# Optimization experiments

Hardware: AMD Instinct MI355X
Metric: run time of the kernel (lower is better)

## Reference

```python
import jax, jax.numpy as jnp
import numpy as np

NUM_HEADS = 12
CF = 2            # compression_factor
DEPTH = 3
BLOCK_DEPTH = 2
TOTAL_DEPTH_M1 = 14 - 1


def setup_inputs() -> dict:
    key = jax.random.key(0)
    k1, k2, k3, k4 = jax.random.split(key, 4)
    B, N, C = 64, 577, 768
    x = jax.random.normal(k1, (B, N, C), dtype=jnp.float32)
    qkv_w = jax.random.normal(k2, (3 * C, C), dtype=jnp.float32) * (C ** -0.5)
    proj_w = jax.random.normal(k3, (C, C), dtype=jnp.float32) * (C ** -0.5)
    proj_b = jax.random.normal(k4, (C,), dtype=jnp.float32) * 0.02
    return {"x": x, "qkv_w": qkv_w, "proj_w": proj_w, "proj_b": proj_b}


def _attn_branch(xh, qkv_w, proj_w, proj_b, zero_small):
    Bh, N, C = xh.shape
    H = NUM_HEADS
    D = C // H
    scale = D ** -0.5
    # qkv projection (no bias), split into q,k,v of shape [Bh, H, N, D]
    qkv = jnp.einsum('bnc,oc->bno', xh, qkv_w)  # [Bh, N, 3C]
    qkv = qkv.reshape(Bh, N, 3, H, D).transpose(2, 0, 3, 1, 4)  # [3, Bh, H, N, D]
    if zero_small:
        # statically zero compressed heads in q, k, v (as the torch in-place write does)
        qkv = qkv.at[:, :, H // CF:].set(0.0)
    q, k, v = qkv[0], qkv[1], qkv[2]
    attn = jnp.einsum('bhnd,bhmd->bhnm', q, k) * scale
    attn = jax.nn.softmax(attn, axis=-1)
    out = jnp.einsum('bhnm,bhmd->bhnd', attn, v)
    out = out.transpose(0, 2, 1, 3).reshape(Bh, N, C)
    out = jnp.einsum('bnc,oc->bno', out, proj_w) + proj_b
    if zero_small:
        out = out.at[:, :, C // CF:].set(0.0)
    return out


def reference(x, qkv_w, proj_w, proj_b):
    B = x.shape[0]
    x_large = _attn_branch(x[:B // 2], qkv_w, proj_w, proj_b, zero_small=False)
    if BLOCK_DEPTH <= DEPTH <= TOTAL_DEPTH_M1 - BLOCK_DEPTH:
        x_small = _attn_branch(x[B // 2:], qkv_w, proj_w, proj_b, zero_small=True)
        return jnp.concatenate((x_large, x_small), axis=0)
    return jnp.concatenate((x_large, x_large), axis=0)
```

## Files before the change

kernel.cpp:

```cpp
#include <hip/hip_runtime.h>

#define BATCH 64
#define SEQ   577
#define CDIM  768
#define NH    12
#define HD    64
#define MROWS (BATCH * SEQ)
#define KDIM  768
#define QKV_N (3 * CDIM)
#define NPAD  640
#define TQ    128
#define PS    40
#define OS    72
#define DEAD_M 18464

typedef short bf16x8 __attribute__((ext_vector_type(8)));
typedef float f32x4  __attribute__((ext_vector_type(4)));

__device__ __forceinline__ unsigned short f2bf(float f) {
  unsigned int u = __float_as_uint(f);
  u += 0x7fffu + ((u >> 16) & 1u);
  return (unsigned short)(u >> 16);
}

__device__ __forceinline__ void async_ld16(const unsigned short* g, unsigned short* l) {
  __builtin_amdgcn_global_load_lds((const __attribute__((address_space(1))) void*)g,
                                   (__attribute__((address_space(3))) void*)l, 16, 0, 0);
}

__device__ __forceinline__ int xcd_swz(int id, int nwg) {
  int q = nwg >> 3, r = nwg & 7;
  int xcd = id & 7, lin = id >> 3;
  int base = (xcd < r) ? xcd * (q + 1) : r * (q + 1) + (xcd - r) * q;
  return base + lin;
}

__global__ __launch_bounds__(256) void cvt_bf16(const float* __restrict__ in,
                                                unsigned short* __restrict__ out, int n4) {
  int i = blockIdx.x * 256 + threadIdx.x;
  if (i < n4) {
    float4 f = ((const float4*)in)[i];
    ushort4 o = make_ushort4(f2bf(f.x), f2bf(f.y), f2bf(f.z), f2bf(f.w));
    ((ushort4*)out)[i] = o;
  }
}

__device__ __forceinline__ void gemm256_loop(
    const unsigned short* __restrict__ A,
    const unsigned short* __restrict__ Bm,
    unsigned short* sL,
    int row0, int col0,
    f32x4 (&acc)[8][4]) {
  const int tid = threadIdx.x;
  const int w = tid >> 6, lane = tid & 63;
  const int quad = lane >> 4, l16 = lane & 15;
  const int wm = w >> 2, wn = w & 3;

  const int rl0 = w * 32 + (lane >> 2);
  const int rl1 = rl0 + 16;
  const int ch = (((lane & 3) ^ ((lane >> 3) & 3)) << 3);
  int ga0 = row0 + rl0; if (ga0 >= MROWS) ga0 = MROWS - 1;
  int ga1 = row0 + rl1; if (ga1 >= MROWS) ga1 = MROWS - 1;
  const unsigned short* aSrc0 = A + (size_t)ga0 * KDIM + ch;
  const unsigned short* aSrc1 = A + (size_t)ga1 * KDIM + ch;
  const unsigned short* bSrc0 = Bm + (size_t)(col0 + rl0) * KDIM + ch;
  const unsigned short* bSrc1 = Bm + (size_t)(col0 + rl1) * KDIM + ch;
  const int sdst = w * 1024;

  const int swz = ((quad ^ ((l16 >> 1) & 3)) << 3);
  const int arow = (wm * 128 + l16) * 32 + swz;
  const int brow = (wn * 64 + l16) * 32 + swz + 16384;

#define STAGE_A(off, kt, ks) do {                                              \
    async_ld16(aSrc0 + (kt) * 64 + (ks) * 32, sL + (off) + (ks) * 8192 + sdst);       \
    async_ld16(aSrc1 + (kt) * 64 + (ks) * 32, sL + (off) + (ks) * 8192 + sdst + 512); \
  } while (0)
#define STAGE_B(off, kt, ks) do {                                              \
    async_ld16(bSrc0 + (kt) * 64 + (ks) * 32, sL + (off) + 16384 + (ks) * 8192 + sdst);       \
    async_ld16(bSrc1 + (kt) * 64 + (ks) * 32, sL + (off) + 16384 + (ks) * 8192 + sdst + 512); \
  } while (0)

  STAGE_A(0, 0, 0); STAGE_B(0, 0, 0); STAGE_A(0, 0, 1); STAGE_B(0, 0, 1);
  asm volatile("s_waitcnt vmcnt(4)" ::: "memory");
  __builtin_amdgcn_s_barrier();

  bf16x8 af[4], bfv[4];
  #pragma unroll 2
  for (int t = 0; t < 12; ++t) {
    const int d = (t & 1) << 15;
    const int nd = d ^ 32768;
    const bool pre = (t < 11);
    #pragma unroll
    for (int i = 0; i < 4; ++i) af[i] = *(const bf16x8*)&sL[d + arow + i * 512];
    #pragma unroll
    for (int j = 0; j < 4; ++j) bfv[j] = *(const bf16x8*)&sL[d + brow + j * 512];
    if (pre) STAGE_A(nd, t + 1, 0);
    __builtin_amdgcn_s_barrier();
    asm volatile("s_waitcnt lgkmcnt(0)" ::: "memory");
    __builtin_amdgcn_sched_barrier(0);
    __builtin_amdgcn_s_setprio(1);
    #pragma unroll
    for (int i = 0; i < 4; ++i)
      #pragma unroll
      for (int j = 0; j < 4; ++j)
        acc[i][j] = __builtin_amdgcn_mfma_f32_16x16x32_bf16(af[i], bfv[j], acc[i][j], 0, 0, 0);
    __builtin_amdgcn_s_setprio(0);
    __builtin_amdgcn_sched_barrier(0);
    __builtin_amdgcn_s_barrier();
    #pragma unroll
    for (int i = 0; i < 4; ++i) af[i] = *(const bf16x8*)&sL[d + arow + (4 + i) * 512];
    if (pre) STAGE_B(nd, t + 1, 0);
    __builtin_amdgcn_s_barrier();
    asm volatile("s_waitcnt lgkmcnt(0)" ::: "memory");
    __builtin_amdgcn_sched_barrier(0);
    __builtin_amdgcn_s_setprio(1);
    #pragma unroll
    for (int i = 0; i < 4; ++i)
      #pragma unroll
      for (int j = 0; j < 4; ++j)
        acc[4 + i][j] = __builtin_amdgcn_mfma_f32_16x16x32_bf16(af[i], bfv[j], acc[4 + i][j], 0, 0, 0);
    __builtin_amdgcn_s_setprio(0);
    __builtin_amdgcn_sched_barrier(0);
    if (pre) asm volatile("s_waitcnt vmcnt(4)" ::: "memory");
    else     asm volatile("s_waitcnt vmcnt(0)" ::: "memory");
    __builtin_amdgcn_s_barrier();
    #pragma unroll
    for (int i = 0; i < 4; ++i) af[i] = *(const bf16x8*)&sL[d + 8192 + arow + i * 512];
    #pragma unroll
    for (int j = 0; j < 4; ++j) bfv[j] = *(const bf16x8*)&sL[d + 8192 + brow + j * 512];
    if (pre) STAGE_A(nd, t + 1, 1);
    __builtin_amdgcn_s_barrier();
    asm volatile("s_waitcnt lgkmcnt(0)" ::: "memory");
    __builtin_amdgcn_sched_barrier(0);
    __builtin_amdgcn_s_setprio(1);
    #pragma unroll
    for (int i = 0; i < 4; ++i)
      #pragma unroll
      for (int j = 0; j < 4; ++j)
        acc[i][j] = __builtin_amdgcn_mfma_f32_16x16x32_bf16(af[i], bfv[j], acc[i][j], 0, 0, 0);
    __builtin_amdgcn_s_setprio(0);
    __builtin_amdgcn_sched_barrier(0);
    __builtin_amdgcn_s_barrier();
    #pragma unroll
    for (int i = 0; i < 4; ++i) af[i] = *(const bf16x8*)&sL[d + 8192 + arow + (4 + i) * 512];
    if (pre) STAGE_B(nd, t + 1, 1);
    __builtin_amdgcn_s_barrier();
    asm volatile("s_waitcnt lgkmcnt(0)" ::: "memory");
    __builtin_amdgcn_sched_barrier(0);
    __builtin_amdgcn_s_setprio(1);
    #pragma unroll
    for (int i = 0; i < 4; ++i)
      #pragma unroll
      for (int j = 0; j < 4; ++j)
        acc[4 + i][j] = __builtin_amdgcn_mfma_f32_16x16x32_bf16(af[i], bfv[j], acc[4 + i][j], 0, 0, 0);
    __builtin_amdgcn_s_setprio(0);
    __builtin_amdgcn_sched_barrier(0);
    if (pre) asm volatile("s_waitcnt vmcnt(4)" ::: "memory");
    __builtin_amdgcn_s_barrier();
  }
#undef STAGE_A
#undef STAGE_B
}

__global__ __launch_bounds__(512, 2) void gemm_qkv(
    const unsigned short* __restrict__ A,
    const unsigned short* __restrict__ Bm,
    unsigned short* __restrict__ qb,
    unsigned short* __restrict__ kb,
    unsigned short* __restrict__ vb) {
  const int wg = xcd_swz(blockIdx.x, 145 * 9);
  const int mt = wg / 9, nt = wg - mt * 9;
  const int row0 = mt * 256, col0 = nt * 256;
  if (row0 >= DEAD_M && (col0 % CDIM) == 512) return;

  __shared__ unsigned short sL[65536];
  f32x4 acc[8][4] = {};
  gemm256_loop(A, Bm, sL, row0, col0, acc);

  const int tid = threadIdx.x;
  const int w = tid >> 6, lane = tid & 63;
  const int quad = lane >> 4, l16 = lane & 15;
  const int wm = w >> 2, wn = w & 3;

  const int wcol = col0 + wn * 64;
  const int three = wcol / CDIM;
  const int rem = wcol - three * CDIM;
  const int h = rem >> 6;
  unsigned short* dst = (three == 0) ? qb : (three == 1) ? kb : vb;
  const float sc = (three == 0) ? 0.180336878f : 1.0f;
  if ((row0 + wm * 128) >= DEAD_M && h >= 6) return;

  unsigned short* so = sL + w * 8192;
  #pragma unroll
  for (int mf = 0; mf < 8; ++mf)
    #pragma unroll
    for (int nf = 0; nf < 4; ++nf)
      #pragma unroll
      for (int r = 0; r < 4; ++r) {
        int rr = mf * 16 + quad * 4 + r;
        so[rr * 64 + (((nf * 2 + (l16 >> 3)) ^ (rr & 7)) << 3) + (l16 & 7)] =
            f2bf(acc[mf][nf][r] * sc);
      }
  #pragma unroll
  for (int it = 0; it < 16; ++it) {
    int c = it * 64 + lane;
    int rr = c >> 3, s8 = c & 7;
    int m = row0 + wm * 128 + rr;
    if (m < MROWS) {
      int b = m / SEQ, n = m - b * SEQ;
      *(int4*)&dst[((((size_t)b * NH + h) * SEQ + n) << 6) + s8 * 8] =
          *(const int4*)&so[rr * 64 + ((s8 ^ (rr & 7)) << 3)];
    }
  }
}

__global__ __launch_bounds__(512) void transpose_v(
    const unsigned short* __restrict__ v,
    unsigned short* __restrict__ vt) {
  const int bh = blockIdx.y;
  const int b = bh / NH, h = bh - b * NH;
  if (b >= 32 && h >= 6) return;
  const int t = blockIdx.x;
  const int tid = threadIdx.x;
  const int w = tid >> 6, lane = tid & 63;
  int n = t * 64 + lane;
  bf16x8 vv = {};
  if (n < SEQ)
    vv = *(const bf16x8*)&v[(size_t)bh * (SEQ * HD) + n * HD + w * 8];
  unsigned short* dst = vt + (size_t)bh * (HD * NPAD) + (w * 8) * NPAD + t * 64 + lane;
  #pragma unroll
  for (int j = 0; j < 8; j++)
    dst[j * NPAD] = ((const unsigned short*)&vv)[j];
}

__global__ __launch_bounds__(256, 4) void flash_attn(
    const unsigned short* __restrict__ q,
    const unsigned short* __restrict__ k,
    const unsigned short* __restrict__ vt,
    unsigned short* __restrict__ attn) {
  const int id = blockIdx.x;
  const int bh8 = id / 40;
  const int rem = id - bh8 * 40;
  const int qt = rem >> 3;
  const int bh = bh8 * 8 + (rem & 7);
  const int b = bh / NH, h = bh - b * NH;
  const int tid = threadIdx.x;
  const int w = tid >> 6, lane = tid & 63;
  const int quad = lane >> 4, l16 = lane & 15;

  if (b >= 32 && h >= 6) {
    for (int it = tid; it < TQ * 8; it += 256) {
      int r = it >> 3, c8 = (it & 7) * 8;
      int n = qt * TQ + r;
      if (n < SEQ)
        *(int4*)&attn[(b * SEQ + n) * CDIM + h * 64 + c8] = make_int4(0, 0, 0, 0);
    }
    return;
  }

  __shared__ unsigned short sK[2 * 64 * 32];
  __shared__ unsigned short sVt[2 * 64 * 32];
  __shared__ unsigned short sP[4][64 * PS];

  const unsigned short* qbase = q + (size_t)bh * (SEQ * HD);
  const unsigned short* kbase = k + (size_t)bh * (SEQ * HD);
  const unsigned short* vtbase = vt + (size_t)bh * (HD * NPAD);

  const int fsw = ((quad ^ ((l16 >> 1) & 3)) << 3);

  bf16x8 aq[2][2];
  #pragma unroll
  for (int g = 0; g < 2; g++) {
    int qr = qt * TQ + w * 32 + g * 16 + l16;
    if (qr > SEQ - 1) qr = SEQ - 1;
    aq[g][0] = *(const bf16x8*)&qbase[qr * HD + quad * 8];
    aq[g][1] = *(const bf16x8*)&qbase[qr * HD + 32 + quad * 8];
  }

  f32x4 oacc[2][4] = {};
  f32x4 lacc[2] = {};

  const short ONE = (short)0x3F80;

  for (int t = 0; t < 10; t++) {
    __syncthreads();
    #pragma unroll
    for (int c = 0; c < 2; c++) {
      int rI = tid >> 2;
      int c4s = (tid & 3) ^ ((tid >> 3) & 3);
      int base = c * 2048 + (tid & ~63) * 8;
      int kr = t * 64 + rI; if (kr > SEQ - 1) kr = SEQ - 1;
      async_ld16(kbase + kr * HD + c * 32 + c4s * 8, sK + base);
      async_ld16(vtbase + rI * NPAD + t * 64 + c * 32 + c4s * 8, sVt + base);
    }
    __syncthreads();

    bf16x8 bk[4][2];
    #pragma unroll
    for (int nt = 0; nt < 4; nt++) {
      bk[nt][0] = *(const bf16x8*)&sK[0 * 2048 + (nt * 16 + l16) * 32 + fsw];
      bk[nt][1] = *(const bf16x8*)&sK[1 * 2048 + (nt * 16 + l16) * 32 + fsw];
    }

    bf16x8 ones0, ones1;
    if (t < 9) {
      #pragma unroll
      for (int j = 0; j < 8; j++) { ones0[j] = ONE; ones1[j] = ONE; }
    } else {
      bf16x8 z = {};
      ones0 = z; ones1 = z;
      ones0[0] = (quad == 0) ? ONE : (short)0;
    }

    #pragma unroll
    for (int g = 0; g < 2; g++) {
      f32x4 s[4];
      #pragma unroll
      for (int nt = 0; nt < 4; nt++) {
        f32x4 z = {};
        z = __builtin_amdgcn_mfma_f32_16x16x32_bf16(aq[g][0], bk[nt][0], z, 0, 0, 0);
        z = __builtin_amdgcn_mfma_f32_16x16x32_bf16(aq[g][1], bk[nt][1], z, 0, 0, 0);
        s[nt] = z;
      }
      #pragma unroll
      for (int nt = 0; nt < 4; nt++)
        #pragma unroll
        for (int r = 0; r < 4; r++)
          sP[w][((g * 2 + (nt >> 1)) * 16 + quad * 4 + r) * PS + (nt & 1) * 16 + l16] =
              f2bf(__builtin_exp2f(s[nt][r]));
    }

    #pragma unroll
    for (int g = 0; g < 2; g++) {
      bf16x8 pa0 = *(const bf16x8*)&sP[w][((g * 2 + 0) * 16 + l16) * PS + quad * 8];
      bf16x8 pa1 = *(const bf16x8*)&sP[w][((g * 2 + 1) * 16 + l16) * PS + quad * 8];
      #pragma unroll
      for (int dt = 0; dt < 4; dt++) {
        bf16x8 bv0 = *(const bf16x8*)&sVt[0 * 2048 + (dt * 16 + l16) * 32 + fsw];
        bf16x8 bv1 = *(const bf16x8*)&sVt[1 * 2048 + (dt * 16 + l16) * 32 + fsw];
        oacc[g][dt] = __builtin_amdgcn_mfma_f32_16x16x32_bf16(pa0, bv0, oacc[g][dt], 0, 0, 0);
        oacc[g][dt] = __builtin_amdgcn_mfma_f32_16x16x32_bf16(pa1, bv1, oacc[g][dt], 0, 0, 0);
      }
      lacc[g] = __builtin_amdgcn_mfma_f32_16x16x32_bf16(pa0, ones0, lacc[g], 0, 0, 0);
      lacc[g] = __builtin_amdgcn_mfma_f32_16x16x32_bf16(pa1, ones1, lacc[g], 0, 0, 0);
    }
  }

  unsigned short* so = &sP[w][0];
  #pragma unroll
  for (int g = 0; g < 2; g++)
    #pragma unroll
    for (int r = 0; r < 4; r++) {
      float inv = 1.0f / lacc[g][r];
      #pragma unroll
      for (int dt = 0; dt < 4; dt++)
        so[(g * 16 + quad * 4 + r) * OS + dt * 16 + l16] = f2bf(oacc[g][dt][r] * inv);
    }
  #pragma unroll
  for (int it = 0; it < 4; it++) {
    int chunk = it * 64 + lane;
    int row = chunk >> 3, c8 = chunk & 7;
    int n = qt * TQ + w * 32 + row;
    if (n < SEQ)
      *(int4*)&attn[(b * SEQ + n) * CDIM + h * 64 + c8 * 8] =
          *(const int4*)&so[row * OS + c8 * 8];
  }
}

__global__ __launch_bounds__(512, 2) void gemm_proj(
    const unsigned short* __restrict__ A,
    const unsigned short* __restrict__ Bm,
    const float* __restrict__ bias,
    float* __restrict__ out) {
  const int wg = xcd_swz(blockIdx.x, 145 * 3);
  const int mt = wg / 3, nt = wg - mt * 3;
  const int row0 = mt * 256, col0 = nt * 256;
  const int tid = threadIdx.x;

  if (row0 >= DEAD_M && col0 >= (CDIM / 2)) {
    float4 z4 = make_float4(0.f, 0.f, 0.f, 0.f);
    #pragma unroll
    for (int it = 0; it < 32; ++it) {
      int idx = it * 512 + tid;
      int r = idx >> 6, c4 = idx & 63;
      int m = row0 + r;
      if (m < MROWS)
        *(float4*)&out[(size_t)m * CDIM + col0 + c4 * 4] = z4;
    }
    return;
  }

  __shared__ unsigned short sL[65536];
  f32x4 acc[8][4] = {};
  gemm256_loop(A, Bm, sL, row0, col0, acc);

  const int w = tid >> 6, lane = tid & 63;
  const int quad = lane >> 4, l16 = lane & 15;
  const int wm = w >> 2, wn = w & 3;

  float bv[4];
  #pragma unroll
  for (int nf = 0; nf < 4; ++nf) bv[nf] = bias[col0 + wn * 64 + nf * 16 + l16];

  #pragma unroll
  for (int mf = 0; mf < 8; ++mf) {
    int mb = row0 + wm * 128 + mf * 16 + quad * 4;
    #pragma unroll
    for (int nf = 0; nf < 4; ++nf) {
      int col = col0 + wn * 64 + nf * 16 + l16;
      bool maskc = (col >= (CDIM / 2));
      #pragma unroll
      for (int r = 0; r < 4; ++r) {
        int m = mb + r;
        if (m < MROWS) {
          float val = acc[mf][nf][r] + bv[nf];
          if (m >= DEAD_M && maskc) val = 0.f;
          out[(size_t)m * CDIM + col] = val;
        }
      }
    }
  }
}

extern "C" void kernel_launch(void* const* d_in, const int* in_sizes, int n_in,
                              void* d_out, int out_size, void* d_ws, size_t ws_size,
                              hipStream_t stream) {
  const float* x      = (const float*)d_in[0];
  const float* qkv_w  = (const float*)d_in[1];
  const float* proj_w = (const float*)d_in[2];
  const float* proj_b = (const float*)d_in[3];
  float* out = (float*)d_out;

  size_t off = 0;
  auto alloc = [&](size_t bytes) {
    void* p = (char*)d_ws + off;
    off += (bytes + 255) & ~(size_t)255;
    return p;
  };
  const size_t XE = (size_t)MROWS * KDIM;
  unsigned short* xb   = (unsigned short*)alloc(XE * 2);
  unsigned short* wqb  = (unsigned short*)alloc((size_t)QKV_N * KDIM * 2);
  unsigned short* wpb  = (unsigned short*)alloc((size_t)CDIM * KDIM * 2);
  unsigned short* qb   = (unsigned short*)alloc(XE * 2);
  unsigned short* kb   = (unsigned short*)alloc(XE * 2);
  unsigned short* vb   = (unsigned short*)alloc(XE * 2);
  unsigned short* vtb  = (unsigned short*)alloc((size_t)BATCH * NH * HD * NPAD * 2);
  unsigned short* attnb = xb;
  (void)ws_size;

  cvt_bf16<<<(int)(XE / 4 / 256), 256, 0, stream>>>(x, xb, (int)(XE / 4));
  cvt_bf16<<<(QKV_N * KDIM / 4) / 256, 256, 0, stream>>>(qkv_w, wqb, QKV_N * KDIM / 4);
  cvt_bf16<<<(CDIM * KDIM / 4) / 256, 256, 0, stream>>>(proj_w, wpb, CDIM * KDIM / 4);

  gemm_qkv<<<dim3(145 * 9), 512, 0, stream>>>(xb, wqb, qb, kb, vb);

  transpose_v<<<dim3(10, BATCH * NH), 512, 0, stream>>>(vb, vtb);

  flash_attn<<<(BATCH * NH / 8) * 40, 256, 0, stream>>>(qb, kb, vtb, attnb);

  gemm_proj<<<dim3(145 * 3), 512, 0, stream>>>(attnb, wpb, proj_b, out);
}
```

Before: 532.9 us.

## Simplify GEMM main loop to one wait and barrier per K tile

Replaces the finely interleaved 256x256 GEMM loop, which staged sub-tiles between MFMA groups with partial vmcnt waits, several barriers, setprio and sched_barrier, with a simpler double-buffered loop. Each iteration waits for all loads, takes one barrier, issues every async load for the next tile, then runs both k-substeps of MFMAs with no intermediate barriers. A barrier is added after the loop so the epilogue can safely reuse shared memory. This cuts barrier and scheduling overhead and gives the compiler freedom to schedule, but waiting with vmcnt(0) at the top of each iteration loses the finer overlap of loads and compute and raises register pressure from holding more fragments at once. The buffer the next loads write was last read in the previous iteration, and the single barrier separates those reads from the new writes.

```diff
diff --git a/kernel.cpp b/kernel.cpp
--- a/kernel.cpp
+++ b/kernel.cpp
@@ -81,82 +81,38 @@
   } while (0)
 
   STAGE_A(0, 0, 0); STAGE_B(0, 0, 0); STAGE_A(0, 0, 1); STAGE_B(0, 0, 1);
-  asm volatile("s_waitcnt vmcnt(4)" ::: "memory");
-  __builtin_amdgcn_s_barrier();
-
-  bf16x8 af[4], bfv[4];
+
   #pragma unroll 2
   for (int t = 0; t < 12; ++t) {
     const int d = (t & 1) << 15;
     const int nd = d ^ 32768;
-    const bool pre = (t < 11);
-    #pragma unroll
-    for (int i = 0; i < 4; ++i) af[i] = *(const bf16x8*)&sL[d + arow + i * 512];
-    #pragma unroll
-    for (int j = 0; j < 4; ++j) bfv[j] = *(const bf16x8*)&sL[d + brow + j * 512];
-    if (pre) STAGE_A(nd, t + 1, 0);
+    asm volatile("s_waitcnt vmcnt(0)" ::: "memory");
     __builtin_amdgcn_s_barrier();
-    asm volatile("s_waitcnt lgkmcnt(0)" ::: "memory");
-    __builtin_amdgcn_sched_barrier(0);
-    __builtin_amdgcn_s_setprio(1);
-    #pragma unroll
-    for (int i = 0; i < 4; ++i)
-      #pragma unroll
-      for (int j = 0; j < 4; ++j)
-        acc[i][j] = __builtin_amdgcn_mfma_f32_16x16x32_bf16(af[i], bfv[j], acc[i][j], 0, 0, 0);
-    __builtin_amdgcn_s_setprio(0);
-    __builtin_amdgcn_sched_barrier(0);
-    __builtin_amdgcn_s_barrier();
-    #pragma unroll
-    for (int i = 0; i < 4; ++i) af[i] = *(const bf16x8*)&sL[d + arow + (4 + i) * 512];
-    if (pre) STAGE_B(nd, t + 1, 0);
-    __builtin_amdgcn_s_barrier();
-    asm volatile("s_waitcnt lgkmcnt(0)" ::: "memory");
-    __builtin_amdgcn_sched_barrier(0);
-    __builtin_amdgcn_s_setprio(1);
-    #pragma unroll
-    for (int i = 0; i < 4; ++i)
-      #pragma unroll
-      for (int j = 0; j < 4; ++j)
-        acc[4 + i][j] = __builtin_amdgcn_mfma_f32_16x16x32_bf16(af[i], bfv[j], acc[4 + i][j], 0, 0, 0);
-    __builtin_amdgcn_s_setprio(0);
-    __builtin_amdgcn_sched_barrier(0);
-    if (pre) asm volatile("s_waitcnt vmcnt(4)" ::: "memory");
-    else     asm volatile("s_waitcnt vmcnt(0)" ::: "memory");
-    __builtin_amdgcn_s_barrier();
-    #pragma unroll
-    for (int i = 0; i < 4; ++i) af[i] = *(const bf16x8*)&sL[d + 8192 + arow + i * 512];
-    #pragma unroll
-    for (int j = 0; j < 4; ++j) bfv[j] = *(const bf16x8*)&sL[d + 8192 + brow + j * 512];
-    if (pre) STAGE_A(nd, t + 1, 1);
-    __builtin_amdgcn_s_barrier();
-    asm volatile("s_waitcnt lgkmcnt(0)" ::: "memory");
-    __builtin_amdgcn_sched_barrier(0);
-    __builtin_amdgcn_s_setprio(1);
-    #pragma unroll
-    for (int i = 0; i < 4; ++i)
-      #pragma unroll
-      for (int j = 0; j < 4; ++j)
-        acc[i][j] = __builtin_amdgcn_mfma_f32_16x16x32_bf16(af[i], bfv[j], acc[i][j], 0, 0, 0);
-    __builtin_amdgcn_s_setprio(0);
-    __builtin_amdgcn_sched_barrier(0);
-    __builtin_amdgcn_s_barrier();
-    #pragma unroll
-    for (int i = 0; i < 4; ++i) af[i] = *(const bf16x8*)&sL[d + 8192 + arow + (4 + i) * 512];
-    if (pre) STAGE_B(nd, t + 1, 1);
-    __builtin_amdgcn_s_barrier();
-    asm volatile("s_waitcnt lgkmcnt(0)" ::: "memory");
-    __builtin_amdgcn_sched_barrier(0);
-    __builtin_amdgcn_s_setprio(1);
-    #pragma unroll
-    for (int i = 0; i < 4; ++i)
-      #pragma unroll
-      for (int j = 0; j < 4; ++j)
-        acc[4 + i][j] = __builtin_amdgcn_mfma_f32_16x16x32_bf16(af[i], bfv[j], acc[4 + i][j], 0, 0, 0);
-    __builtin_amdgcn_s_setprio(0);
-    __builtin_amdgcn_sched_barrier(0);
-    if (pre) asm volatile("s_waitcnt vmcnt(4)" ::: "memory");
-    __builtin_amdgcn_s_barrier();
+    if (t < 11) {
+      STAGE_A(nd, t + 1, 0); STAGE_B(nd, t + 1, 0);
+      STAGE_A(nd, t + 1, 1); STAGE_B(nd, t + 1, 1);
+    }
+    #pragma unroll
+    for (int ks = 0; ks < 2; ++ks) {
+      const int kb = d + ks * 8192;
+      bf16x8 a0[4], a1[4], bv[4];
+      #pragma unroll
+      for (int i = 0; i < 4; ++i) a0[i] = *(const bf16x8*)&sL[kb + arow + i * 512];
+      #pragma unroll
+      for (int j = 0; j < 4; ++j) bv[j] = *(const bf16x8*)&sL[kb + brow + j * 512];
+      #pragma unroll
+      for (int i = 0; i < 4; ++i) a1[i] = *(const bf16x8*)&sL[kb + arow + (4 + i) * 512];
+      #pragma unroll
+      for (int i = 0; i < 4; ++i)
+        #pragma unroll
+        for (int j = 0; j < 4; ++j)
+          acc[i][j] = __builtin_amdgcn_mfma_f32_16x16x32_bf16(a0[i], bv[j], acc[i][j], 0, 0, 0);
+      #pragma unroll
+      for (int i = 0; i < 4; ++i)
+        #pragma unroll
+        for (int j = 0; j < 4; ++j)
+          acc[4 + i][j] = __builtin_amdgcn_mfma_f32_16x16x32_bf16(a1[i], bv[j], acc[4 + i][j], 0, 0, 0);
+    }
   }
 #undef STAGE_A
 #undef STAGE_B
@@ -176,6 +132,8 @@
   __shared__ unsigned short sL[65536];
   f32x4 acc[8][4] = {};
   gemm256_loop(A, Bm, sL, row0, col0, acc);
+
+  __builtin_amdgcn_s_barrier();
 
   const int tid = threadIdx.x;
   const int w = tid >> 6, lane = tid & 63;
```

Measured after the change: 557.9 us. +4.7%, slower.
